# Optimization experiments

Measured on AMD Instinct MI355X. Metric: run time of the kernel, lower is better.

The kernel has to match this reference:

```python
import jax, jax.numpy as jnp
import numpy as np

N_VIEWS = 2
TEMPERATURE = 0.07


def setup_inputs() -> dict:
    key = jax.random.key(0)
    # concatenated features for n_views=2 views of batch_size=4096, proj dim 128
    features = jax.random.normal(key, (8192, 128), dtype=jnp.float32)
    return {"features": features}


def reference(features) -> jnp.ndarray:
    # NT-Xent / SimCLR loss, faithful to the torch module:
    #   sim = F F^T ; drop diagonal ; logits = [positive, negatives] / T ;
    #   CE with label 0  ==  mean( logsumexp(off_diag/T) - positive/T )
    # (concatenating [pos, neg] is a row permutation of the off-diagonal
    #  entries, and CrossEntropy(label=0) only needs logsumexp(row) - pos.)
    N = features.shape[0]
    B = N // N_VIEWS
    inv_t = 1.0 / TEMPERATURE

    sim = jnp.matmul(features, features.T)  # [N, N]

    row = jnp.arange(N)
    # off-diagonal column indices in increasing-j order, matching mask.view:
    # cols[i] = [0..i-1, i+1..N-1]
    cols = jnp.arange(N - 1)[None, :]
    cols = cols + (cols >= row[:, None])  # [N, N-1]
    sim_offdiag = jnp.take_along_axis(sim, cols, axis=1)  # [N, N-1]

    # with n_views=2 the single positive for row i is its other view (i+B) % N
    pos = sim[row, (row + B) % N]  # [N]

    lse = jax.nn.logsumexp(sim_offdiag * inv_t, axis=1)  # [N]
    loss = jnp.mean(lse - pos * inv_t)
    return loss
```

## Files before the change

### kernel.cpp

```cpp
#include <hip/hip_runtime.h>
#include <math.h>

typedef __bf16 bf16x8 __attribute__((ext_vector_type(8)));
typedef float f32x4 __attribute__((ext_vector_type(4)));
typedef unsigned short u16x8 __attribute__((ext_vector_type(8)));

#define N_TOT 8192
#define HALF_N 4096
#define D 128
#define INV_T 14.285714285714286f
#define CSC 20.609929155556627f
#define NCSC -20.609929155556627f
#define LN2F 0.69314718055994531f
#define NEG_BIG -3.0e38f
#define M_INIT -1.0e30f
#define THR_RAW 1.0f
#define CS 16

__device__ __forceinline__ unsigned short f2bf(float f) {
    union { float f; unsigned int u; } a; a.f = f;
    unsigned int u = a.u;
    return (unsigned short)((u + 0x7fffu + ((u >> 16) & 1u)) >> 16);
}

__global__ __launch_bounds__(256)
void cvt_kernel(const float* __restrict__ in, unsigned short* __restrict__ fbP) {
    const int c   = blockIdx.x * 256 + threadIdx.x;
    const int q   = c >> 6;
    const int rem = c & 63;
    const int lg  = rem >> 4, lr = rem & 15;
    const int kk  = q & 3;
    const int col = (q >> 2) * 16 + lr;
    const int j16 = kk * 4 + lg;
    const float4 v0 = reinterpret_cast<const float4*>(in)[col * 32 + j16 * 2];
    const float4 v1 = reinterpret_cast<const float4*>(in)[col * 32 + j16 * 2 + 1];
    u16x8 o;
    o[0] = f2bf(v0.x); o[1] = f2bf(v0.y); o[2] = f2bf(v0.z); o[3] = f2bf(v0.w);
    o[4] = f2bf(v1.x); o[5] = f2bf(v1.y); o[6] = f2bf(v1.z); o[7] = f2bf(v1.w);
    reinterpret_cast<u16x8*>(fbP)[c] = o;
}

__global__ __launch_bounds__(512, 4)
void simclr_kernel(const unsigned short* __restrict__ fbP,
                   float* __restrict__ pm, float* __restrict__ ps,
                   float* __restrict__ rowpos) {
    const int tid  = threadIdx.x;
    const int lane = tid & 63;
    const int wid  = tid >> 6;
    const int lr   = lane & 15;
    const int lg   = lane >> 4;
    const int RT0  = blockIdx.x * 16 + wid * 2;
    const int Tw   = blockIdx.y * 32;

    auto ld16 = [&](int chunk) -> bf16x8 {
        return *reinterpret_cast<const bf16x8*>(fbP + (size_t)chunk * 8);
    };

    bf16x8 br[2][4];
#pragma unroll
    for (int rt = 0; rt < 2; ++rt)
#pragma unroll
        for (int kk = 0; kk < 4; ++kk)
            br[rt][kk] = ld16(((RT0 + rt) * 4 + kk) * 64 + lane);

    float m[2], s[2];
#pragma unroll
    for (int rt = 0; rt < 2; ++rt) { m[rt] = M_INIT; s[rt] = 0.f; }

    int p = (wid & 3) << 2;
    bf16x8 ca[4], cb[4];
#pragma unroll
    for (int kk = 0; kk < 4; ++kk) ca[kk] = ld16(((Tw + 2 * p) * 4 + kk) * 64 + lane);
#pragma unroll
    for (int kk = 0; kk < 4; ++kk) cb[kk] = ld16(((Tw + 2 * p + 1) * 4 + kk) * 64 + lane);

#pragma unroll 1
    for (int i = 0; i < 16; ++i) {
        const int pn = (p + 1) & 15;
        const int c0 = blockIdx.y * 512 + p * 32;

        f32x4 accP[2], accQ[2];
#pragma unroll
        for (int rt = 0; rt < 2; ++rt) accP[rt] = f32x4{0.f, 0.f, 0.f, 0.f};
        __builtin_amdgcn_s_setprio(1);
#pragma unroll
        for (int kk = 0; kk < 4; ++kk)
#pragma unroll
            for (int rt = 0; rt < 2; ++rt)
                accP[rt] = __builtin_amdgcn_mfma_f32_16x16x32_bf16(ca[kk], br[rt][kk], accP[rt], 0, 0, 0);
        __builtin_amdgcn_s_setprio(0);
        if (i < 15) {
#pragma unroll
            for (int kk = 0; kk < 4; ++kk)
                ca[kk] = ld16(((Tw + 2 * pn) * 4 + kk) * 64 + lane);
        }

#pragma unroll
        for (int rt = 0; rt < 2; ++rt) accQ[rt] = f32x4{0.f, 0.f, 0.f, 0.f};
        __builtin_amdgcn_s_setprio(1);
#pragma unroll
        for (int kk = 0; kk < 4; ++kk)
#pragma unroll
            for (int rt = 0; rt < 2; ++rt)
                accQ[rt] = __builtin_amdgcn_mfma_f32_16x16x32_bf16(cb[kk], br[rt][kk], accQ[rt], 0, 0, 0);
        __builtin_amdgcn_s_setprio(0);
        if (i < 15) {
#pragma unroll
            for (int kk = 0; kk < 4; ++kk)
                cb[kk] = ld16(((Tw + 2 * pn + 1) * 4 + kk) * 64 + lane);
        }

#pragma unroll
        for (int rt = 0; rt < 2; ++rt) {
            const int rowbase = (RT0 + rt) * 16;
            f32x4 P = accP[rt], Q = accQ[rt];
            if (c0 == (rowbase ^ HALF_N)) {
#pragma unroll
                for (int r = 0; r < 4; ++r)
                    if (lr == lg * 4 + r) rowpos[rowbase + lr] = P[r];
            }
            if (c0 + 16 == (rowbase ^ HALF_N)) {
#pragma unroll
                for (int r = 0; r < 4; ++r)
                    if (lr == lg * 4 + r) rowpos[rowbase + lr] = Q[r];
            }
            if (c0 == rowbase) {
#pragma unroll
                for (int r = 0; r < 4; ++r)
                    if (lr == lg * 4 + r) P[r] = NEG_BIG;
            }
            if (c0 + 16 == rowbase) {
#pragma unroll
                for (int r = 0; r < 4; ++r)
                    if (lr == lg * 4 + r) Q[r] = NEG_BIG;
            }
            const float t1 = fmaxf(fmaxf(P[0], P[1]), P[2]);
            const float t2 = fmaxf(fmaxf(P[3], Q[0]), Q[1]);
            const float t3 = fmaxf(Q[2], Q[3]);
            const float rmax = fmaxf(fmaxf(t1, t2), t3);
            if (!__all(rmax <= m[rt] + THR_RAW)) {
                const float mn = fmaxf(m[rt], rmax);
                s[rt] *= __builtin_amdgcn_exp2f(fmaf(m[rt], CSC, mn * NCSC));
                m[rt] = mn;
            }
            const float cm = m[rt] * NCSC;
            const float e0 = __builtin_amdgcn_exp2f(fmaf(P[0], CSC, cm));
            const float e1 = __builtin_amdgcn_exp2f(fmaf(P[1], CSC, cm));
            const float e2 = __builtin_amdgcn_exp2f(fmaf(P[2], CSC, cm));
            const float e3 = __builtin_amdgcn_exp2f(fmaf(P[3], CSC, cm));
            const float e4 = __builtin_amdgcn_exp2f(fmaf(Q[0], CSC, cm));
            const float e5 = __builtin_amdgcn_exp2f(fmaf(Q[1], CSC, cm));
            const float e6 = __builtin_amdgcn_exp2f(fmaf(Q[2], CSC, cm));
            const float e7 = __builtin_amdgcn_exp2f(fmaf(Q[3], CSC, cm));
            s[rt] += ((e0 + e1) + (e2 + e3)) + ((e4 + e5) + (e6 + e7));
        }
        p = pn;
    }

#pragma unroll
    for (int rt = 0; rt < 2; ++rt) {
        float M = m[rt];
        M = fmaxf(M, __shfl_xor(M, 16, 64));
        M = fmaxf(M, __shfl_xor(M, 32, 64));
        float sc = s[rt] * __builtin_amdgcn_exp2f(fmaf(m[rt], CSC, M * NCSC));
        sc += __shfl_xor(sc, 16, 64);
        sc += __shfl_xor(sc, 32, 64);
        if (lg == 0) {
            const int row = (RT0 + rt) * 16 + lr;
            pm[blockIdx.y * N_TOT + row] = M;
            ps[blockIdx.y * N_TOT + row] = sc;
        }
    }
}

__global__ __launch_bounds__(256)
void rowloss_mean_kernel(const float* __restrict__ pm, const float* __restrict__ ps,
                         const float* __restrict__ rowpos, float* __restrict__ out) {
    const int row = blockIdx.x * 256 + threadIdx.x;
    float M = pm[row], S = ps[row];
#pragma unroll
    for (int c = 1; c < CS; ++c) {
        const float Mo = pm[c * N_TOT + row], So = ps[c * N_TOT + row];
        const float mn = fmaxf(M, Mo);
        S = fmaf(S,  __builtin_amdgcn_exp2f(fmaf(M,  CSC, mn * NCSC)),
                 So * __builtin_amdgcn_exp2f(fmaf(Mo, CSC, mn * NCSC)));
        M = mn;
    }
    float acc = LN2F * fmaf(M, CSC, __builtin_amdgcn_logf(S)) - rowpos[row] * INV_T;
#pragma unroll
    for (int off = 32; off > 0; off >>= 1) acc += __shfl_xor(acc, off, 64);
    __shared__ float ls[4];
    if ((threadIdx.x & 63) == 0) ls[threadIdx.x >> 6] = acc;
    __syncthreads();
    if (threadIdx.x == 0)
        atomicAdd(out, (ls[0] + ls[1] + ls[2] + ls[3]) * (1.0f / (float)N_TOT));
}

extern "C" void kernel_launch(void* const* d_in, const int* in_sizes, int n_in,
                              void* d_out, int out_size, void* d_ws, size_t ws_size,
                              hipStream_t stream) {
    const float* feat = (const float*)d_in[0];
    char* ws = (char*)d_ws;
    unsigned short* fbP = (unsigned short*)ws;
    float* pm      = (float*)(ws + (size_t)N_TOT * D * 2);
    float* ps      = (float*)(ws + (size_t)N_TOT * D * 2 + (size_t)CS * N_TOT * 4);
    float* rowpos  = (float*)(ws + (size_t)N_TOT * D * 2 + 2 * (size_t)CS * N_TOT * 4);
    float* out = (float*)d_out;

    hipMemsetAsync(out, 0, sizeof(float), stream);
    cvt_kernel<<<512, 256, 0, stream>>>(feat, fbP);
    simclr_kernel<<<dim3(32, CS), 512, 0, stream>>>(fbP, pm, ps, rowpos);
    rowloss_mean_kernel<<<N_TOT / 256, 256, 0, stream>>>(pm, ps, rowpos, out);
}
```

Before: 43.92 us.

## Stage column tiles through LDS with async double buffering, 4 row tiles per wave

Instead of each wave loading its own column fragments straight from global memory, the block now stages each 32-column tile into a double-buffered LDS region with global_load_lds and all waves read it from there. Blocks shrink to 4 waves, each owning 4 row tiles, so every column fragment feeds twice as many MFMAs and global/L2 traffic drops. The cost is a block barrier per iteration, higher register pressure from 4 row tiles (launch bounds lowered to 3 blocks per CU), and loss of the per-wave staggered column start and setprio hints.

```diff
diff --git a/kernel.cpp b/kernel.cpp
--- a/kernel.cpp
+++ b/kernel.cpp
@@ -40,78 +40,79 @@
     reinterpret_cast<u16x8*>(fbP)[c] = o;
 }
 
-__global__ __launch_bounds__(512, 4)
+__global__ __launch_bounds__(256, 3)
 void simclr_kernel(const unsigned short* __restrict__ fbP,
                    float* __restrict__ pm, float* __restrict__ ps,
                    float* __restrict__ rowpos) {
+    __shared__ __align__(16) unsigned short lds[2][4096];
     const int tid  = threadIdx.x;
     const int lane = tid & 63;
     const int wid  = tid >> 6;
     const int lr   = lane & 15;
     const int lg   = lane >> 4;
-    const int RT0  = blockIdx.x * 16 + wid * 2;
+    const int RT0  = blockIdx.x * 16 + wid * 4;
     const int Tw   = blockIdx.y * 32;
 
-    auto ld16 = [&](int chunk) -> bf16x8 {
-        return *reinterpret_cast<const bf16x8*>(fbP + (size_t)chunk * 8);
+    bf16x8 br[4][4];
+#pragma unroll
+    for (int rt = 0; rt < 4; ++rt)
+#pragma unroll
+        for (int kk = 0; kk < 4; ++kk)
+            br[rt][kk] = *reinterpret_cast<const bf16x8*>(
+                fbP + ((size_t)(((RT0 + rt) * 4 + kk) * 64) + lane) * 8);
+
+    float m[4], s[4];
+#pragma unroll
+    for (int rt = 0; rt < 4; ++rt) { m[rt] = M_INIT; s[rt] = 0.f; }
+
+    auto stage = [&](int p, int b) {
+#pragma unroll
+        for (int h = 0; h < 2; ++h) {
+            const unsigned short* src =
+                fbP + ((size_t)(Tw + 2 * p) * 256 + h * 256 + tid) * 8;
+            unsigned short* dst = &lds[b][(h * 256 + tid) * 8];
+            __builtin_amdgcn_global_load_lds(
+                (const __attribute__((address_space(1))) unsigned int*)(const void*)src,
+                (__attribute__((address_space(3))) unsigned int*)(void*)dst,
+                16, 0, 0);
+        }
     };
 
-    bf16x8 br[2][4];
-#pragma unroll
-    for (int rt = 0; rt < 2; ++rt)
+    stage(0, 0);
+    __syncthreads();
+
+    int buf = 0;
+#pragma unroll 1
+    for (int p = 0; p < 16; ++p) {
+        if (p < 15) stage(p + 1, buf ^ 1);
+
+        bf16x8 ca[4], cb[4];
+#pragma unroll
+        for (int kk = 0; kk < 4; ++kk) {
+            ca[kk] = *reinterpret_cast<const bf16x8*>(&lds[buf][(kk * 64 + lane) * 8]);
+            cb[kk] = *reinterpret_cast<const bf16x8*>(&lds[buf][((kk + 4) * 64 + lane) * 8]);
+        }
+
+        const int c0 = blockIdx.y * 512 + p * 32;
+
+        f32x4 accP[4], accQ[4];
+#pragma unroll
+        for (int rt = 0; rt < 4; ++rt) accP[rt] = f32x4{0.f, 0.f, 0.f, 0.f};
 #pragma unroll
         for (int kk = 0; kk < 4; ++kk)
-            br[rt][kk] = ld16(((RT0 + rt) * 4 + kk) * 64 + lane);
-
-    float m[2], s[2];
-#pragma unroll
-    for (int rt = 0; rt < 2; ++rt) { m[rt] = M_INIT; s[rt] = 0.f; }
-
-    int p = (wid & 3) << 2;
-    bf16x8 ca[4], cb[4];
-#pragma unroll
-    for (int kk = 0; kk < 4; ++kk) ca[kk] = ld16(((Tw + 2 * p) * 4 + kk) * 64 + lane);
-#pragma unroll
-    for (int kk = 0; kk < 4; ++kk) cb[kk] = ld16(((Tw + 2 * p + 1) * 4 + kk) * 64 + lane);
-
-#pragma unroll 1
-    for (int i = 0; i < 16; ++i) {
-        const int pn = (p + 1) & 15;
-        const int c0 = blockIdx.y * 512 + p * 32;
-
-        f32x4 accP[2], accQ[2];
-#pragma unroll
-        for (int rt = 0; rt < 2; ++rt) accP[rt] = f32x4{0.f, 0.f, 0.f, 0.f};
-        __builtin_amdgcn_s_setprio(1);
+#pragma unroll
+            for (int rt = 0; rt < 4; ++rt)
+                accP[rt] = __builtin_amdgcn_mfma_f32_16x16x32_bf16(ca[kk], br[rt][kk], accP[rt], 0, 0, 0);
+#pragma unroll
+        for (int rt = 0; rt < 4; ++rt) accQ[rt] = f32x4{0.f, 0.f, 0.f, 0.f};
 #pragma unroll
         for (int kk = 0; kk < 4; ++kk)
 #pragma unroll
-            for (int rt = 0; rt < 2; ++rt)
-                accP[rt] = __builtin_amdgcn_mfma_f32_16x16x32_bf16(ca[kk], br[rt][kk], accP[rt], 0, 0, 0);
-        __builtin_amdgcn_s_setprio(0);
-        if (i < 15) {
-#pragma unroll
-            for (int kk = 0; kk < 4; ++kk)
-                ca[kk] = ld16(((Tw + 2 * pn) * 4 + kk) * 64 + lane);
-        }
-
-#pragma unroll
-        for (int rt = 0; rt < 2; ++rt) accQ[rt] = f32x4{0.f, 0.f, 0.f, 0.f};
-        __builtin_amdgcn_s_setprio(1);
-#pragma unroll
-        for (int kk = 0; kk < 4; ++kk)
-#pragma unroll
-            for (int rt = 0; rt < 2; ++rt)
+            for (int rt = 0; rt < 4; ++rt)
                 accQ[rt] = __builtin_amdgcn_mfma_f32_16x16x32_bf16(cb[kk], br[rt][kk], accQ[rt], 0, 0, 0);
-        __builtin_amdgcn_s_setprio(0);
-        if (i < 15) {
-#pragma unroll
-            for (int kk = 0; kk < 4; ++kk)
-                cb[kk] = ld16(((Tw + 2 * pn + 1) * 4 + kk) * 64 + lane);
-        }
-
-#pragma unroll
-        for (int rt = 0; rt < 2; ++rt) {
+
+#pragma unroll
+        for (int rt = 0; rt < 4; ++rt) {
             const int rowbase = (RT0 + rt) * 16;
             f32x4 P = accP[rt], Q = accQ[rt];
             if (c0 == (rowbase ^ HALF_N)) {
@@ -154,11 +155,13 @@
             const float e7 = __builtin_amdgcn_exp2f(fmaf(Q[3], CSC, cm));
             s[rt] += ((e0 + e1) + (e2 + e3)) + ((e4 + e5) + (e6 + e7));
         }
-        p = pn;
+
+        __syncthreads();
+        buf ^= 1;
     }
 
 #pragma unroll
-    for (int rt = 0; rt < 2; ++rt) {
+    for (int rt = 0; rt < 4; ++rt) {
         float M = m[rt];
         M = fmaxf(M, __shfl_xor(M, 16, 64));
         M = fmaxf(M, __shfl_xor(M, 32, 64));
@@ -209,6 +212,6 @@
 
     hipMemsetAsync(out, 0, sizeof(float), stream);
     cvt_kernel<<<512, 256, 0, stream>>>(feat, fbP);
-    simclr_kernel<<<dim3(32, CS), 512, 0, stream>>>(fbP, pm, ps, rowpos);
+    simclr_kernel<<<dim3(32, CS), 256, 0, stream>>>(fbP, pm, ps, rowpos);
     rowloss_mean_kernel<<<N_TOT / 256, 256, 0, stream>>>(pm, ps, rowpos, out);
 }
```

After: 42.78 us. 2.6% less time.
